# Performance work log

Measured on AMD Instinct MI355X. Metric: run time of the kernel, lower is better.

## Reference

```python
import jax, jax.numpy as jnp
import numpy as np

LN_EPS = 1e-5  # torch.nn.LayerNorm default

def g(x):
    # minGRU activation: x + 0.5 for x >= 0, sigmoid(x) otherwise (always positive)
    return jnp.where(x >= 0, x + 0.5, jax.nn.sigmoid(x))

def log_g(x):
    return jnp.where(x >= 0, jnp.log(jax.nn.relu(x) + 0.5), -jax.nn.softplus(-x))

def layernorm(x, gamma, beta):
    mu = jnp.mean(x, axis=-1, keepdims=True)
    var = jnp.var(x, axis=-1, keepdims=True)
    return (x - mu) * jax.lax.rsqrt(var + LN_EPS) * gamma + beta

def mingru_scan(gate, hidden, h0):
    # gate, hidden: (B,S,D); h0: (B,1,D) positive
    # z = sigmoid(gate); h_t = (1-z_t)*h_{t-1} + z_t * g(hidden_t)
    # evaluated via Heinsen parallel scan in log space
    log_z = -jax.nn.softplus(-gate)          # log sigmoid(gate)
    log_coeffs = -jax.nn.softplus(gate)      # log(1 - sigmoid(gate))
    log_h0 = jnp.log(h0)                     # (B,1,D)
    log_tilde_h = log_g(hidden)
    a_star = jnp.cumsum(
        jnp.concatenate([jnp.zeros_like(log_h0), log_coeffs], axis=1), axis=1
    )                                        # (B,S+1,D)
    log_vals = jnp.concatenate([log_h0, log_z + log_tilde_h], axis=1) - a_star
    log_h = a_star + jax.lax.cumlogsumexp(log_vals, axis=1)
    return jnp.exp(log_h)[:, 1:]             # (B,S,D)

def setup_inputs() -> dict:
    key = jax.random.key(0)
    k1, k2 = jax.random.split(key)
    B, S, D, L = 8, 4096, 1024, 3
    x = jax.random.normal(k1, (B, S, D), dtype=jnp.float32)
    W = jax.random.normal(k2, (L, D, 2 * D), dtype=jnp.float32) * 0.02
    b = jnp.zeros((L, 2 * D), dtype=jnp.float32)
    ln_gamma = jnp.ones((L, D), dtype=jnp.float32)
    ln_beta = jnp.zeros((L, D), dtype=jnp.float32)
    return {"x": x, "ln_gamma": ln_gamma, "ln_beta": ln_beta, "W": W, "b": b}

def reference(x, ln_gamma, ln_beta, W, b):
    B, S, D = x.shape
    L = W.shape[0]
    inp = x
    next_hidden = []
    for l in range(L):
        h_prev = jnp.full((B, 1, D), 0.5, dtype=x.dtype)  # g(zeros) = 0.5
        xn = layernorm(inp, ln_gamma[l], ln_beta[l])
        gh = jnp.einsum('bsd,de->bse', xn, W[l]) + b[l]   # (B,S,2D)
        gate, hidden = jnp.split(gh, 2, axis=2)
        out = mingru_scan(gate, hidden, h_prev)
        next_hidden.append(out[:, -1:])
        out = out + inp  # residual (sizes equal -> identity res_align)
        inp = out
    return (out, *next_hidden)
```

## Files before the change

### kernel.cpp

```cpp
#include <hip/hip_runtime.h>

typedef unsigned short u16;
typedef unsigned int   u32;
typedef float  f32x4  __attribute__((ext_vector_type(4)));
typedef short  bf16x8 __attribute__((ext_vector_type(8)));
typedef u16    u16x4  __attribute__((ext_vector_type(4)));

#define BQ 8
#define SQ 4096
#define DQ 1024
#define NQ 2048
#define MQ 32768
#define KQ 1024
#define CCH 64
#define TCH 64
#define NT 16

__device__ __forceinline__ float bf2f(u16 u){
  union { u32 i; float f; } v; v.i = ((u32)u) << 16; return v.f;
}
__device__ __forceinline__ u16 f2bf(float f){
  union { float f; u32 i; } v; v.f = f;
  u32 r = v.i + 0x7fffu + ((v.i >> 16) & 1u);
  return (u16)(r >> 16);
}

__device__ __forceinline__ void sig_ab(float gate, float hid, float& a, float& bv){
  float eg = __expf(gate);
  float a_ = __builtin_amdgcn_rcpf(1.f + eg);
  float z  = 1.f - a_;
  float eh = __expf(hid);
  float sg = eh * __builtin_amdgcn_rcpf(1.f + eh);
  float gval = (hid >= 0.f) ? (hid + 0.5f) : sg;
  a = a_; bv = z * gval;
}

__device__ __forceinline__ void gload_lds16(const u16* g, u16* l){
  __builtin_amdgcn_global_load_lds(
      (const __attribute__((address_space(1))) u32*)g,
      (__attribute__((address_space(3)))       u32*)l,
      16, 0, 0);
}

__global__ __launch_bounds__(256) void wt_cast(const float* __restrict__ W,
                                               u16* __restrict__ WT){
  __shared__ float t[64][65];
  const int l  = blockIdx.z;
  const int k0 = blockIdx.x << 6, n0 = blockIdx.y << 6;
  const float* Wl = W  + (size_t)l * KQ * NQ;
  u16*         Tl = WT + (size_t)l * NQ * KQ;
  const int c = threadIdx.x & 63, r4 = threadIdx.x >> 6;
  #pragma unroll
  for (int i = 0; i < 16; ++i){
    int r = i * 4 + r4;
    t[r][c] = Wl[(size_t)(k0 + r) * NQ + n0 + c];
  }
  __syncthreads();
  #pragma unroll
  for (int i = 0; i < 16; ++i){
    int r = i * 4 + r4;
    Tl[(size_t)(n0 + r) * KQ + k0 + c] = f2bf(t[c][r]);
  }
}

__global__ __launch_bounds__(256) void ln_cast(const float* __restrict__ x,
                                               const float* __restrict__ gamma,
                                               const float* __restrict__ beta,
                                               u16* __restrict__ xn){
  const size_t row = blockIdx.x;
  const int tid = threadIdx.x;
  f32x4 xv = *(const f32x4*)(x + row * DQ + tid * 4);
  float s  = xv[0] + xv[1] + xv[2] + xv[3];
  float s2 = xv[0]*xv[0] + xv[1]*xv[1] + xv[2]*xv[2] + xv[3]*xv[3];
  #pragma unroll
  for (int off = 32; off > 0; off >>= 1){
    s  += __shfl_down(s,  off);
    s2 += __shfl_down(s2, off);
  }
  __shared__ float red[8];
  const int wave = tid >> 6, lane = tid & 63;
  if (lane == 0){ red[wave] = s; red[4 + wave] = s2; }
  __syncthreads();
  s  = red[0] + red[1] + red[2] + red[3];
  s2 = red[4] + red[5] + red[6] + red[7];
  const float mean = s * (1.f / DQ);
  float var = fmaxf(s2 * (1.f / DQ) - mean * mean, 0.f);
  const float rstd = rsqrtf(var + 1e-5f);
  f32x4 gv = *(const f32x4*)(gamma + tid * 4);
  f32x4 bv = *(const f32x4*)(beta  + tid * 4);
  u16x4 o;
  #pragma unroll
  for (int e = 0; e < 4; ++e) o[e] = f2bf((xv[e] - mean) * rstd * gv[e] + bv[e]);
  *(u16x4*)(xn + row * DQ + tid * 4) = o;
}

__global__ __launch_bounds__(512, 2) void gemm_k8(const u16* __restrict__ A,
                                                  const u16* __restrict__ Bt,
                                                  const float* __restrict__ bias,
                                                  u16* __restrict__ Cg){
  __shared__ u16 lds[2][2][2][8192];
  const int bid = blockIdx.x;
  const int swz = ((bid & 7) << 7) | (bid >> 3);
  const int bn = swz & 7, bm = swz >> 3;
  const int n0 = bn << 8, m0 = bm << 8;
  const int tid = threadIdx.x;
  const int w = tid >> 6, lane = tid & 63;
  const int wr = w >> 2, wc = w & 3;
  const int lr = lane & 15, hi = lane >> 4;
  const int sl8 = lane >> 3;
  const int sslot = (lane & 7) ^ sl8;

  f32x4 acc[2][2][4][2] = {};
  bf16x8 afr[4][2];
  bf16x8 bf0[2][2], bf1[2][2];

#define FENCE asm volatile("" ::: "memory")
#define BAR do { FENCE; __builtin_amdgcn_s_barrier(); FENCE; } while(0)

#define STAGE(op, hf, kt, pb_) do {                                             \
    const u16* gsrc_ = (op) ? Bt : A;                                           \
    const int rb_ = ((op) ? n0 : m0) + ((hf) << 7);                             \
    _Pragma("unroll")                                                           \
    for (int g_ = 0; g_ < 2; ++g_){                                             \
      const int row_ = (w << 4) + (g_ << 3) + sl8;                              \
      gload_lds16(gsrc_ + (size_t)(rb_ + row_) * KQ + ((kt) << 6) + (sslot << 3),\
                  &lds[pb_][op][hf][((w << 4) + (g_ << 3)) << 6]);              \
    }                                                                           \
  } while(0)

#define LDSRD(dst, base_, row_, slot_) do {                                     \
    const int r_ = (row_);                                                      \
    dst = *(const bf16x8*)((const char*)(base_) +                               \
          ((r_ << 7) + ((((slot_)) ^ (r_ & 7)) << 4)));                         \
  } while(0)

#define RD_A(hf) do {                                                           \
    const u16* Ah_ = &lds[pb][0][hf][0];                                        \
    _Pragma("unroll")                                                           \
    for (int i_ = 0; i_ < 4; ++i_)                                              \
      _Pragma("unroll")                                                         \
      for (int kk_ = 0; kk_ < 2; ++kk_)                                         \
        LDSRD(afr[i_][kk_], Ah_, (wr << 6) + (i_ << 4) + lr, (kk_ << 2) + hi);  \
  } while(0)

#define RD_B(dst, hf) do {                                                      \
    const u16* Bh_ = &lds[pb][1][hf][0];                                        \
    _Pragma("unroll")                                                           \
    for (int j_ = 0; j_ < 2; ++j_)                                              \
      _Pragma("unroll")                                                         \
      for (int kk_ = 0; kk_ < 2; ++kk_)                                         \
        LDSRD(dst[j_][kk_], Bh_, (wc << 5) + (j_ << 4) + lr, (kk_ << 2) + hi);  \
  } while(0)

#define MM(qm, qn, B) do {                                                      \
    _Pragma("unroll")                                                           \
    for (int i_ = 0; i_ < 4; ++i_)                                              \
      _Pragma("unroll")                                                         \
      for (int j_ = 0; j_ < 2; ++j_)                                            \
        _Pragma("unroll")                                                       \
        for (int kk_ = 0; kk_ < 2; ++kk_)                                       \
          acc[qm][qn][i_][j_] = __builtin_amdgcn_mfma_f32_16x16x32_bf16(        \
              afr[i_][kk_], B[j_][kk_], acc[qm][qn][i_][j_], 0, 0, 0);          \
  } while(0)

#define PH(RDS, STG, MFMAS, VMW) do {                                           \
    RDS;                                                                        \
    STG;                                                                        \
    BAR;                                                                        \
    asm volatile("s_waitcnt lgkmcnt(0)" ::: "memory");                          \
    __builtin_amdgcn_s_setprio(1);                                              \
    MFMAS;                                                                      \
    __builtin_amdgcn_s_setprio(0);                                              \
    VMW;                                                                        \
    BAR;                                                                        \
  } while(0)

  STAGE(0, 0, 0, 0); STAGE(0, 1, 0, 0); STAGE(1, 0, 0, 0); STAGE(1, 1, 0, 0);
  STAGE(0, 0, 1, 1); STAGE(1, 0, 1, 1);
  asm volatile("s_waitcnt vmcnt(4)" ::: "memory");
  BAR;

  for (int t = 0; t < NT; ++t){
    const int pb = t & 1, qb = pb ^ 1;
    const bool s1 = (t + 1 < NT), s2 = (t + 2 < NT);
    PH(RD_A(0); RD_B(bf0, 0), if (s1) STAGE(0, 1, t + 1, qb), MM(0, 0, bf0), );
    PH(RD_B(bf1, 1),          if (s1) STAGE(1, 1, t + 1, qb), MM(0, 1, bf1), );
    PH(RD_A(1),               if (s2) STAGE(0, 0, t + 2, pb), MM(1, 0, bf0), );
    PH(,                      if (s2) STAGE(1, 0, t + 2, pb), MM(1, 1, bf1),
       if (s2) { asm volatile("s_waitcnt vmcnt(4)" ::: "memory"); }
       else    { asm volatile("s_waitcnt vmcnt(0)" ::: "memory"); });
  }
#undef PH
#undef MM
#undef RD_B
#undef RD_A
#undef LDSRD
#undef STAGE

  #pragma unroll
  for (int qn = 0; qn < 2; ++qn)
    #pragma unroll
    for (int j = 0; j < 2; ++j){
      const int col = n0 + (qn << 7) + (wc << 5) + (j << 4) + lr;
      const float bj = bias[col];
      #pragma unroll
      for (int qm = 0; qm < 2; ++qm)
        #pragma unroll
        for (int i = 0; i < 4; ++i){
          const int row0 = m0 + (qm << 7) + (wr << 6) + (i << 4) + (hi << 2);
          #pragma unroll
          for (int r = 0; r < 4; ++r)
            Cg[(size_t)(row0 + r) * NQ + col] = f2bf(acc[qm][qn][i][j][r] + bj);
        }
    }
#undef BAR
#undef FENCE
}

__global__ __launch_bounds__(256) void scan1(const u16* __restrict__ gh,
                                             float* __restrict__ P,
                                             float* __restrict__ Q){
  const int b = blockIdx.x >> 6;
  const int c = blockIdx.x & 63;
  const int d4 = threadIdx.x << 2;
  const u16* base = gh + ((size_t)(b * SQ + c * TCH) * NQ) + d4;
  float p[4] = {1.f,1.f,1.f,1.f}, q[4] = {0.f,0.f,0.f,0.f};
  for (int t = 0; t < TCH; ++t){
    u16x4 gv = *(const u16x4*)(base + (size_t)t * NQ);
    u16x4 hv = *(const u16x4*)(base + (size_t)t * NQ + DQ);
    #pragma unroll
    for (int e = 0; e < 4; ++e){
      float a, bv; sig_ab(bf2f(gv[e]), bf2f(hv[e]), a, bv);
      p[e] *= a; q[e] = a * q[e] + bv;
    }
  }
  const size_t o = ((size_t)blockIdx.x << 10) + d4;
  *(f32x4*)(P + o) = f32x4{p[0], p[1], p[2], p[3]};
  *(f32x4*)(Q + o) = f32x4{q[0], q[1], q[2], q[3]};
}

__global__ __launch_bounds__(256) void scan2(const float* __restrict__ P,
                                             const float* __restrict__ Q,
                                             float* __restrict__ hst,
                                             float* __restrict__ hlast){
  const int idx = blockIdx.x * 256 + threadIdx.x;
  const int b = idx >> 10, d = idx & 1023;
  float h = 0.5f;
  for (int c = 0; c < CCH; ++c){
    const size_t o = ((size_t)(b * CCH + c) << 10) + d;
    hst[o] = h;
    h = P[o] * h + Q[o];
  }
  hlast[idx] = h;
}

__global__ __launch_bounds__(256) void scan3(const u16* __restrict__ gh,
                                             const float* __restrict__ hst,
                                             const float* __restrict__ inp,
                                             float* __restrict__ outp){
  const int b = blockIdx.x >> 6;
  const int c = blockIdx.x & 63;
  const int d4 = threadIdx.x << 2;
  const size_t srow = (size_t)(b * SQ + c * TCH);
  const u16*   base = gh   + srow * NQ + d4;
  const float* ib   = inp  + srow * DQ + d4;
  float*       ob   = outp + srow * DQ + d4;
  const size_t o = ((size_t)blockIdx.x << 10) + d4;
  f32x4 h0 = *(const f32x4*)(hst + o);
  float h[4] = {h0[0], h0[1], h0[2], h0[3]};
  for (int t = 0; t < TCH; ++t){
    u16x4 gv = *(const u16x4*)(base + (size_t)t * NQ);
    u16x4 hh = *(const u16x4*)(base + (size_t)t * NQ + DQ);
    f32x4 iv = *(const f32x4*)(ib + (size_t)t * DQ);
    f32x4 ov;
    #pragma unroll
    for (int e = 0; e < 4; ++e){
      float a, bv; sig_ab(bf2f(gv[e]), bf2f(hh[e]), a, bv);
      h[e] = a * h[e] + bv;
      ov[e] = h[e] + iv[e];
    }
    *(f32x4*)(ob + (size_t)t * DQ) = ov;
  }
}

extern "C" void kernel_launch(void* const* d_in, const int* in_sizes, int n_in,
                              void* d_out, int out_size, void* d_ws, size_t ws_size,
                              hipStream_t stream) {
  const float* x     = (const float*)d_in[0];
  const float* gamma = (const float*)d_in[1];
  const float* beta  = (const float*)d_in[2];
  const float* W     = (const float*)d_in[3];
  const float* bias  = (const float*)d_in[4];
  float* out = (float*)d_out;

  char* ws = (char*)d_ws;
  const size_t ACT = (size_t)MQ * DQ * 4;
  float* bufA = (float*)(ws);
  float* bufB = (float*)(ws + ACT);
  u16*   gh   = (u16*)  (ws + 2 * ACT);
  u16*   xn   = (u16*)  (ws + 3 * ACT);
  u16*   WT   = (u16*)  (ws + 3 * ACT + (size_t)MQ * DQ * 2);
  float* Pa   = (float*)(ws + 3 * ACT + (size_t)MQ * DQ * 2 + (size_t)3 * NQ * KQ * 2);
  float* Qa   = Pa + (size_t)BQ * CCH * DQ;
  float* hst  = Qa + (size_t)BQ * CCH * DQ;

  wt_cast<<<dim3(KQ / 64, NQ / 64, 3), 256, 0, stream>>>(W, WT);

  const float* inp = x;
  for (int l = 0; l < 3; ++l){
    ln_cast<<<MQ, 256, 0, stream>>>(inp, gamma + l * DQ, beta + l * DQ, xn);
    gemm_k8<<<dim3((NQ / 256) * (MQ / 256)), 512, 0, stream>>>(
        xn, WT + (size_t)l * NQ * KQ, bias + l * NQ, gh);
    scan1<<<BQ * CCH, 256, 0, stream>>>(gh, Pa, Qa);
    scan2<<<(BQ * DQ) / 256, 256, 0, stream>>>(Pa, Qa, hst, out + (size_t)MQ * DQ + l * BQ * DQ);
    float* o = (l == 2) ? out : (l == 0 ? bufA : bufB);
    scan3<<<BQ * CCH, 256, 0, stream>>>(gh, hst, inp, o);
    inp = o;
  }
}
```

Baseline: 866.0 us.

## Fuse next-layer LayerNorm into scan3, store residual in bf16, re-pipeline GEMM staging

The scan3 kernel now also computes the LayerNorm of its output rows and writes the bf16 normalized input for the next layer, which removes two standalone ln_cast launches. The intermediate residual activations are kept in bf16 instead of fp32, halving their traffic. This adds a per-timestep block reduction and __syncthreads inside the scan loop and loses precision on the residual stream. Separately, the GEMM main loop is reorganised to wait on vmcnt and barrier before staging, with a single-step-ahead prefetch replacing the two-deep staging.

Measured after the change: 814.5 us. 1.06x faster.

```diff
diff --git a/kernel.cpp b/kernel.cpp
--- a/kernel.cpp
+++ b/kernel.cpp
@@ -163,32 +163,40 @@
               afr[i_][kk_], B[j_][kk_], acc[qm][qn][i_][j_], 0, 0, 0);          \
   } while(0)
 
-#define PH(RDS, STG, MFMAS, VMW) do {                                           \
+#define PH(VMW, STG, RDS, MFMAS) do {                                           \
+    VMW;                                                                        \
+    BAR;                                                                        \
+    STG;                                                                        \
     RDS;                                                                        \
-    STG;                                                                        \
-    BAR;                                                                        \
     asm volatile("s_waitcnt lgkmcnt(0)" ::: "memory");                          \
     __builtin_amdgcn_s_setprio(1);                                              \
     MFMAS;                                                                      \
     __builtin_amdgcn_s_setprio(0);                                              \
-    VMW;                                                                        \
-    BAR;                                                                        \
-  } while(0)
-
-  STAGE(0, 0, 0, 0); STAGE(0, 1, 0, 0); STAGE(1, 0, 0, 0); STAGE(1, 1, 0, 0);
-  STAGE(0, 0, 1, 1); STAGE(1, 0, 1, 1);
-  asm volatile("s_waitcnt vmcnt(4)" ::: "memory");
-  BAR;
+  } while(0)
+
+  STAGE(1, 0, 0, 0); STAGE(0, 0, 0, 0); STAGE(1, 1, 0, 0); STAGE(0, 1, 0, 0);
 
   for (int t = 0; t < NT; ++t){
     const int pb = t & 1, qb = pb ^ 1;
-    const bool s1 = (t + 1 < NT), s2 = (t + 2 < NT);
-    PH(RD_A(0); RD_B(bf0, 0), if (s1) STAGE(0, 1, t + 1, qb), MM(0, 0, bf0), );
-    PH(RD_B(bf1, 1),          if (s1) STAGE(1, 1, t + 1, qb), MM(0, 1, bf1), );
-    PH(RD_A(1),               if (s2) STAGE(0, 0, t + 2, pb), MM(1, 0, bf0), );
-    PH(,                      if (s2) STAGE(1, 0, t + 2, pb), MM(1, 1, bf1),
-       if (s2) { asm volatile("s_waitcnt vmcnt(4)" ::: "memory"); }
-       else    { asm volatile("s_waitcnt vmcnt(0)" ::: "memory"); });
+    const bool s = (t + 1 < NT);
+    PH(asm volatile("s_waitcnt vmcnt(4)" ::: "memory"),
+       if (s) STAGE(1, 0, t + 1, qb),
+       RD_A(0); RD_B(bf0, 0),
+       MM(0, 0, bf0));
+    PH(if (s) { asm volatile("s_waitcnt vmcnt(4)" ::: "memory"); }
+       else   { asm volatile("s_waitcnt vmcnt(2)" ::: "memory"); },
+       if (s) STAGE(0, 0, t + 1, qb),
+       RD_B(bf1, 1),
+       MM(0, 1, bf1));
+    PH(if (s) { asm volatile("s_waitcnt vmcnt(4)" ::: "memory"); }
+       else   { asm volatile("s_waitcnt vmcnt(0)" ::: "memory"); },
+       if (s) STAGE(1, 1, t + 1, qb),
+       RD_A(1),
+       MM(1, 0, bf0));
+    PH(,
+       if (s) STAGE(0, 1, t + 1, qb),
+       ,
+       MM(1, 1, bf1));
   }
 #undef PH
 #undef MM
@@ -254,32 +262,76 @@
   hlast[idx] = h;
 }
 
-__global__ __launch_bounds__(256) void scan3(const u16* __restrict__ gh,
-                                             const float* __restrict__ hst,
-                                             const float* __restrict__ inp,
-                                             float* __restrict__ outp){
+template<int MODE>
+__global__ __launch_bounds__(256) void scan3f(const u16* __restrict__ gh,
+                                              const float* __restrict__ hst,
+                                              const void* __restrict__ inp,
+                                              void* __restrict__ outp,
+                                              u16* __restrict__ xn,
+                                              const float* __restrict__ gamma,
+                                              const float* __restrict__ beta){
   const int b = blockIdx.x >> 6;
   const int c = blockIdx.x & 63;
-  const int d4 = threadIdx.x << 2;
+  const int tid = threadIdx.x;
+  const int d4 = tid << 2;
+  const int wave = tid >> 6, lane = tid & 63;
   const size_t srow = (size_t)(b * SQ + c * TCH);
-  const u16*   base = gh   + srow * NQ + d4;
-  const float* ib   = inp  + srow * DQ + d4;
-  float*       ob   = outp + srow * DQ + d4;
+  const u16* base = gh + srow * NQ + d4;
   const size_t o = ((size_t)blockIdx.x << 10) + d4;
-  f32x4 h0 = *(const f32x4*)(hst + o);
-  float h[4] = {h0[0], h0[1], h0[2], h0[3]};
+  f32x4 h0v = *(const f32x4*)(hst + o);
+  float h[4] = {h0v[0], h0v[1], h0v[2], h0v[3]};
+  __shared__ float red[2][8];
+  f32x4 gv = {}, bvv = {};
+  if (MODE != 2){
+    gv  = *(const f32x4*)(gamma + d4);
+    bvv = *(const f32x4*)(beta  + d4);
+  }
   for (int t = 0; t < TCH; ++t){
-    u16x4 gv = *(const u16x4*)(base + (size_t)t * NQ);
+    u16x4 gg = *(const u16x4*)(base + (size_t)t * NQ);
     u16x4 hh = *(const u16x4*)(base + (size_t)t * NQ + DQ);
-    f32x4 iv = *(const f32x4*)(ib + (size_t)t * DQ);
+    f32x4 iv;
+    if (MODE == 0){
+      iv = *(const f32x4*)((const float*)inp + (srow + t) * DQ + d4);
+    } else {
+      u16x4 ib = *(const u16x4*)((const u16*)inp + (srow + t) * DQ + d4);
+      #pragma unroll
+      for (int e = 0; e < 4; ++e) iv[e] = bf2f(ib[e]);
+    }
     f32x4 ov;
     #pragma unroll
     for (int e = 0; e < 4; ++e){
-      float a, bv; sig_ab(bf2f(gv[e]), bf2f(hh[e]), a, bv);
+      float a, bv; sig_ab(bf2f(gg[e]), bf2f(hh[e]), a, bv);
       h[e] = a * h[e] + bv;
       ov[e] = h[e] + iv[e];
     }
-    *(f32x4*)(ob + (size_t)t * DQ) = ov;
+    if (MODE == 2){
+      *(f32x4*)((float*)outp + (srow + t) * DQ + d4) = ov;
+    } else {
+      u16x4 ob;
+      #pragma unroll
+      for (int e = 0; e < 4; ++e) ob[e] = f2bf(ov[e]);
+      *(u16x4*)((u16*)outp + (srow + t) * DQ + d4) = ob;
+      float s  = ov[0] + ov[1] + ov[2] + ov[3];
+      float s2 = ov[0]*ov[0] + ov[1]*ov[1] + ov[2]*ov[2] + ov[3]*ov[3];
+      #pragma unroll
+      for (int off = 32; off > 0; off >>= 1){
+        s  += __shfl_down(s,  off);
+        s2 += __shfl_down(s2, off);
+      }
+      const int rb = t & 1;
+      if (lane == 0){ red[rb][wave] = s; red[rb][4 + wave] = s2; }
+      __syncthreads();
+      s  = red[rb][0] + red[rb][1] + red[rb][2] + red[rb][3];
+      s2 = red[rb][4] + red[rb][5] + red[rb][6] + red[rb][7];
+      const float mean = s * (1.f / DQ);
+      float var = fmaxf(s2 * (1.f / DQ) - mean * mean, 0.f);
+      const float rstd = rsqrtf(var + 1e-5f);
+      u16x4 xo;
+      #pragma unroll
+      for (int e = 0; e < 4; ++e)
+        xo[e] = f2bf((ov[e] - mean) * rstd * gv[e] + bvv[e]);
+      *(u16x4*)(xn + (srow + t) * DQ + d4) = xo;
+    }
   }
 }
 
@@ -295,8 +347,8 @@
 
   char* ws = (char*)d_ws;
   const size_t ACT = (size_t)MQ * DQ * 4;
-  float* bufA = (float*)(ws);
-  float* bufB = (float*)(ws + ACT);
+  u16*   bufA = (u16*)(ws);
+  u16*   bufB = (u16*)(ws + ACT);
   u16*   gh   = (u16*)  (ws + 2 * ACT);
   u16*   xn   = (u16*)  (ws + 3 * ACT);
   u16*   WT   = (u16*)  (ws + 3 * ACT + (size_t)MQ * DQ * 2);
@@ -306,15 +358,24 @@
 
   wt_cast<<<dim3(KQ / 64, NQ / 64, 3), 256, 0, stream>>>(W, WT);
 
-  const float* inp = x;
-  for (int l = 0; l < 3; ++l){
-    ln_cast<<<MQ, 256, 0, stream>>>(inp, gamma + l * DQ, beta + l * DQ, xn);
-    gemm_k8<<<dim3((NQ / 256) * (MQ / 256)), 512, 0, stream>>>(
-        xn, WT + (size_t)l * NQ * KQ, bias + l * NQ, gh);
-    scan1<<<BQ * CCH, 256, 0, stream>>>(gh, Pa, Qa);
-    scan2<<<(BQ * DQ) / 256, 256, 0, stream>>>(Pa, Qa, hst, out + (size_t)MQ * DQ + l * BQ * DQ);
-    float* o = (l == 2) ? out : (l == 0 ? bufA : bufB);
-    scan3<<<BQ * CCH, 256, 0, stream>>>(gh, hst, inp, o);
-    inp = o;
-  }
-}
+  ln_cast<<<MQ, 256, 0, stream>>>(x, gamma, beta, xn);
+  gemm_k8<<<dim3((NQ / 256) * (MQ / 256)), 512, 0, stream>>>(xn, WT, bias, gh);
+  scan1<<<BQ * CCH, 256, 0, stream>>>(gh, Pa, Qa);
+  scan2<<<(BQ * DQ) / 256, 256, 0, stream>>>(Pa, Qa, hst, out + (size_t)MQ * DQ);
+  scan3f<0><<<BQ * CCH, 256, 0, stream>>>(gh, hst, x, bufA, xn,
+                                          gamma + DQ, beta + DQ);
+  gemm_k8<<<dim3((NQ / 256) * (MQ / 256)), 512, 0, stream>>>(
+      xn, WT + (size_t)NQ * KQ, bias + NQ, gh);
+  scan1<<<BQ * CCH, 256, 0, stream>>>(gh, Pa, Qa);
+  scan2<<<(BQ * DQ) / 256, 256, 0, stream>>>(Pa, Qa, hst,
+                                             out + (size_t)MQ * DQ + BQ * DQ);
+  scan3f<1><<<BQ * CCH, 256, 0, stream>>>(gh, hst, bufA, bufB, xn,
+                                          gamma + 2 * DQ, beta + 2 * DQ);
+  gemm_k8<<<dim3((NQ / 256) * (MQ / 256)), 512, 0, stream>>>(
+      xn, WT + (size_t)2 * NQ * KQ, bias + 2 * NQ, gh);
+  scan1<<<BQ * CCH, 256, 0, stream>>>(gh, Pa, Qa);
+  scan2<<<(BQ * DQ) / 256, 256, 0, stream>>>(Pa, Qa, hst,
+                                             out + (size_t)MQ * DQ + 2 * BQ * DQ);
+  scan3f<2><<<BQ * CCH, 256, 0, stream>>>(gh, hst, bufB, out, nullptr,
+                                          nullptr, nullptr);
+}
```
